# Performance work log

Measured on AMD Instinct MI355X. Metric: run time of the kernel, lower is better.

The kernel has to match this reference:

```python
import jax, jax.numpy as jnp
import numpy as np

TWO_PI = 2.0 * np.pi
EPS = 1e-6


def radians_to_Q(psi, alpha, eta):
    # returns [N,3,3] with columns gamma_1, gamma_2, gamma_3
    ca, sa = jnp.cos(alpha), jnp.sin(alpha)
    ce, se = jnp.cos(eta), jnp.sin(eta)
    cp, sp = jnp.cos(psi), jnp.sin(psi)
    g1 = jnp.stack([ca, sa * ce, sa * se], axis=-1)
    g2 = jnp.stack([-cp * sa, cp * ca * ce - sp * se, cp * ca * se + sp * ce], axis=-1)
    g3 = jnp.stack([sp * sa, -sp * ca * ce - cp * se, -sp * ca * se + cp * ce], axis=-1)
    return jnp.stack([g1, g2, g3], axis=-1)  # [N,3,3], columns are gammas


def log_approximate_c(kappa, beta):
    product = (kappa - 2 * beta) * (kappa + 2 * beta) + EPS
    return jnp.log(TWO_PI) + kappa - 0.5 * jnp.log(product)


def log_del_kappa(kappa, beta):
    num = jnp.log(-TWO_PI * (4 * beta ** 2 + kappa - kappa ** 2)) + kappa
    den = 1.5 * jnp.log(kappa - 2 * beta) + 1.5 * jnp.log(kappa + 2 * beta) + EPS
    return num - den


def log_del_2_kappa(kappa, beta):
    num = jnp.log(TWO_PI * (kappa ** 4 - 2 * kappa ** 3 + (2 - 8 * beta ** 2) * kappa ** 2
                            + 8 * beta ** 2 * kappa + 16 * beta ** 4 + 4 * beta ** 2)) + kappa
    den = 2.5 * jnp.log(kappa - 2 * beta) + 2.5 * jnp.log(kappa + 2 * beta) + EPS
    return num - den


def expected_x(gamma_a1, c, c_k):
    return jnp.exp(c_k - c)[:, None] * gamma_a1  # [N,3]


def expected_xxT(kappa, beta, Q, c, c_k):
    c_kk = log_del_2_kappa(kappa, beta)
    c_beta = log_del_beta(kappa, beta)
    l1 = jnp.exp(c_k - c)
    l2 = 0.5 * (1 - jnp.exp(c_kk - c) + jnp.exp(c_beta - c))
    l3 = 0.5 * (1 - jnp.exp(c_kk - c) - jnp.exp(c_beta - c))
    lam = jnp.stack([l1, l2, l3], axis=-1)  # [N,3]
    # Q diag(lam) Q^T
    return jnp.einsum('nij,nj,nkj->nik', Q, lam, Q)


def log_del_beta(kappa, beta):
    num = jnp.log(8 * np.pi * kappa) + jnp.log(beta)
    den = 1.5 * jnp.log(kappa - 2 * beta) + 1.5 * jnp.log(kappa + 2 * beta) + EPS
    return num - den


def beta_terms(beta_a, gamma_a2, beta_b, gamma_b2, ExxT_a):
    # term_a: beta_a * gamma_a2^T ExxT_a gamma_a2, broadcast over M
    qa = jnp.einsum('ni,nij,nj->n', gamma_a2, ExxT_a, gamma_a2)  # [N]
    term_a = (beta_a * qa)[:, None]  # [N,1] -> broadcast to [N,M]
    # term_b: beta_b * gamma_b2^T ExxT_a gamma_b2 pairwise
    qb = jnp.einsum('mi,nij,mj->nm', gamma_b2, ExxT_a, gamma_b2)  # [N,M]
    term_b = beta_b[None, :] * qb
    M = beta_b.shape[0]
    return jnp.broadcast_to(term_a, (beta_a.shape[0], M)), term_b


def kappa_term(kappa_a, gamma_a1, kappa_b, gamma_b1, Ex_a):
    ka = kappa_a[:, None] * gamma_a1  # [N,3]
    kb = kappa_b[:, None] * gamma_b1  # [M,3]
    # sum over d of (ka[n]-kb[m]) * Ex_a[n]
    return jnp.einsum('nd,nd->n', ka, Ex_a)[:, None] - jnp.einsum('md,nd->nm', kb, Ex_a)


def get_kld(kent_pred, kent_target):
    eta_a, alpha_a, psi_a, kappa_a, beta_a = [kent_pred[:, i] for i in range(5)]
    eta_b, alpha_b, psi_b, kappa_b, beta_b = [kent_target[:, i] for i in range(5)]

    Qa = radians_to_Q(psi_a, alpha_a, eta_a)  # [N,3,3]
    Qb = radians_to_Q(psi_b, alpha_b, eta_b)  # [M,3,3]
    gamma_a1, gamma_a2, gamma_a3 = Qa[:, :, 0], Qa[:, :, 1], Qa[:, :, 2]
    gamma_b1, gamma_b2, gamma_b3 = Qb[:, :, 0], Qb[:, :, 1], Qb[:, :, 2]

    c_a = log_approximate_c(kappa_a, beta_a)
    c_b = log_approximate_c(kappa_b, beta_b)
    c_ka = log_del_kappa(kappa_a, beta_a)

    Ex_a = expected_x(gamma_a1, c_a, c_ka)
    ExxT_a = expected_xxT(kappa_a, beta_a, Qa, c_a, c_ka)

    log_term = c_b[None, :] - c_a[:, None]
    ex_a_term = kappa_term(kappa_a, gamma_a1, kappa_b, gamma_b1, Ex_a)
    ba1, bb1 = beta_terms(beta_a, gamma_a2, beta_b, gamma_b2, ExxT_a)
    ba2, bb2 = beta_terms(beta_a, gamma_a3, beta_b, gamma_b3, ExxT_a)
    return log_term + ex_a_term + ba1 - bb1 - ba2 + bb2


def _make_kent(key, n):
    k1, k2, k3, k4, k5 = jax.random.split(key, 5)
    eta = jax.random.uniform(k1, (n,), minval=-np.pi, maxval=np.pi)
    alpha = jax.random.uniform(k2, (n,), minval=0.0, maxval=np.pi)
    psi = jax.random.uniform(k3, (n,), minval=-np.pi, maxval=np.pi)
    kappa = jax.random.uniform(k4, (n,), minval=10.0, maxval=50.0)
    beta = 0.2 * kappa * jax.random.uniform(k5, (n,), minval=0.5, maxval=1.0)
    return jnp.stack([eta, alpha, psi, kappa, beta], axis=1).astype(jnp.float32)


def setup_inputs() -> dict:
    key = jax.random.key(0)
    kp, kt = jax.random.split(key)
    N = 2048
    M = 2048
    return {"kent_pred": _make_kent(kp, N), "kent_target": _make_kent(kt, M)}


def reference(kent_pred, kent_target):
    return get_kld(kent_pred, kent_target)
```

## Files before the change

kernel.cpp:

```cpp
#include <hip/hip_runtime.h>
#include <math.h>

#define TWO_PI_F 6.2831853071795864769f
#define EPS_F 1e-6f
#define PI_F 3.14159265358979323846f

__device__ __forceinline__ void kent_frame(float eta, float alpha, float psi,
                                           float& g1x, float& g1y, float& g1z,
                                           float& g2x, float& g2y, float& g2z,
                                           float& g3x, float& g3y, float& g3z) {
    float ca = cosf(alpha), sa = sinf(alpha);
    float ce = cosf(eta),   se = sinf(eta);
    float cp = cosf(psi),   sp = sinf(psi);
    g1x = ca;        g1y = sa * ce;                  g1z = sa * se;
    g2x = -cp * sa;  g2y = cp * ca * ce - sp * se;   g2z = cp * ca * se + sp * ce;
    g3x = sp * sa;   g3y = -sp * ca * ce - cp * se;  g3z = -sp * ca * se + cp * ce;
}

__global__ __launch_bounds__(256) void kent_precompute(
    const float* __restrict__ pred, const float* __restrict__ targ,
    float* __restrict__ fw, float* __restrict__ gw, int N, int M)
{
    int i = blockIdx.x * blockDim.x + threadIdx.x;
    if (i < N) {
        const float* r = pred + (size_t)i * 5;
        float eta = r[0], alpha = r[1], psi = r[2], kap = r[3], bet = r[4];
        float g1x,g1y,g1z,g2x,g2y,g2z,g3x,g3y,g3z;
        kent_frame(eta, alpha, psi, g1x,g1y,g1z, g2x,g2y,g2z, g3x,g3y,g3z);

        float km = kap - 2.f*bet, kp = kap + 2.f*bet;
        float lkm = logf(km), lkp = logf(kp);
        float c   = logf(TWO_PI_F) + kap - 0.5f*logf(km*kp + EPS_F);
        float b2 = bet*bet;
        float ck  = logf(TWO_PI_F*(kap*kap - kap - 4.f*b2)) + kap
                  - (1.5f*lkm + 1.5f*lkp + EPS_F);
        float k2 = kap*kap;
        float poly = k2*k2 - 2.f*kap*k2 + (2.f - 8.f*b2)*k2 + 8.f*b2*kap
                   + 16.f*b2*b2 + 4.f*b2;
        float ckk = logf(TWO_PI_F*poly) + kap - (2.5f*lkm + 2.5f*lkp + EPS_F);
        float cbt = logf(8.f*PI_F*kap) + logf(bet) - (1.5f*lkm + 1.5f*lkp + EPS_F);

        float l1  = expf(ck  - c);
        float ekk = expf(ckk - c);
        float eb  = expf(cbt - c);
        float l2 = 0.5f*(1.f - ekk + eb);
        float l3 = 0.5f*(1.f - ekk - eb);

        float Ex = l1*g1x, Ey = l1*g1y, Ez = l1*g1z;
        float S00 = l1*g1x*g1x + l2*g2x*g2x + l3*g3x*g3x;
        float S11 = l1*g1y*g1y + l2*g2y*g2y + l3*g3y*g3y;
        float S22 = l1*g1z*g1z + l2*g2z*g2z + l3*g3z*g3z;
        float S01 = l1*g1x*g1y + l2*g2x*g2y + l3*g3x*g3y;
        float S02 = l1*g1x*g1z + l2*g2x*g2z + l3*g3x*g3z;
        float S12 = l1*g1y*g1z + l2*g2y*g2z + l3*g3y*g3z;

        float qa2 = S00*g2x*g2x + S11*g2y*g2y + S22*g2z*g2z
                  + 2.f*(S01*g2x*g2y + S02*g2x*g2z + S12*g2y*g2z);
        float qa3 = S00*g3x*g3x + S11*g3y*g3y + S22*g3z*g3z
                  + 2.f*(S01*g3x*g3y + S02*g3x*g3z + S12*g3y*g3z);
        float dg1Ex = g1x*Ex + g1y*Ey + g1z*Ez;
        float A = -c + kap*dg1Ex + bet*(qa2 - qa3);

        float* f = fw + (size_t)i * 10;
        f[0]=Ex; f[1]=Ey; f[2]=Ez;
        f[3]=S00; f[4]=S11; f[5]=S22;
        f[6]=2.f*S01; f[7]=2.f*S02; f[8]=2.f*S12;
        f[9]=A;
    } else if (i < N + M) {
        int m = i - N;
        const float* r = targ + (size_t)m * 5;
        float eta = r[0], alpha = r[1], psi = r[2], kap = r[3], bet = r[4];
        float g1x,g1y,g1z,g2x,g2y,g2z,g3x,g3y,g3z;
        kent_frame(eta, alpha, psi, g1x,g1y,g1z, g2x,g2y,g2z, g3x,g3y,g3z);

        float km = kap - 2.f*bet, kp = kap + 2.f*bet;
        float cB = logf(TWO_PI_F) + kap - 0.5f*logf(km*kp + EPS_F);

        float D00 = g2x*g2x - g3x*g3x;
        float D11 = g2y*g2y - g3y*g3y;
        float D22 = g2z*g2z - g3z*g3z;
        float D01 = g2x*g2y - g3x*g3y;
        float D02 = g2x*g2z - g3x*g3z;
        float D12 = g2y*g2z - g3y*g3z;

        gw[0*(size_t)M + m] = kap*g1x;
        gw[1*(size_t)M + m] = kap*g1y;
        gw[2*(size_t)M + m] = kap*g1z;
        gw[3*(size_t)M + m] = bet*D00;
        gw[4*(size_t)M + m] = bet*D11;
        gw[5*(size_t)M + m] = bet*D22;
        gw[6*(size_t)M + m] = bet*D01;
        gw[7*(size_t)M + m] = bet*D02;
        gw[8*(size_t)M + m] = bet*D12;
        gw[9*(size_t)M + m] = cB;
    }
}

__global__ __launch_bounds__(256) void kent_kld_main(
    const float* __restrict__ fw, const float* __restrict__ gw,
    float* __restrict__ out, int N, int M)
{
    int t = threadIdx.x;
    int m0 = blockIdx.x * 1024 + t * 4;
    int n0 = blockIdx.y * 8;
    if (m0 >= M) return;

    if (m0 + 3 < M) {
        float4 G[10];
#pragma unroll
        for (int k = 0; k < 10; ++k)
            G[k] = *(const float4*)(&gw[(size_t)k * M + m0]);
#pragma unroll
        for (int rr = 0; rr < 8; ++rr) {
            int n = n0 + rr;
            if (n >= N) break;
            const float* f = fw + (size_t)n * 10;
            float A = f[9];
            float4 o;
            o.x = A + G[9].x; o.y = A + G[9].y;
            o.z = A + G[9].z; o.w = A + G[9].w;
#pragma unroll
            for (int k = 0; k < 9; ++k) {
                float fk = f[k];
                o.x = fmaf(-fk, G[k].x, o.x);
                o.y = fmaf(-fk, G[k].y, o.y);
                o.z = fmaf(-fk, G[k].z, o.z);
                o.w = fmaf(-fk, G[k].w, o.w);
            }
            *(float4*)(&out[(size_t)n * M + m0]) = o;
        }
    } else {
        for (int mm = m0; mm < M; ++mm) {
            for (int rr = 0; rr < 8; ++rr) {
                int n = n0 + rr;
                if (n >= N) break;
                const float* f = fw + (size_t)n * 10;
                float acc = f[9] + gw[9*(size_t)M + mm];
                for (int k = 0; k < 9; ++k)
                    acc = fmaf(-f[k], gw[(size_t)k * M + mm], acc);
                out[(size_t)n * M + mm] = acc;
            }
        }
    }
}

extern "C" void kernel_launch(void* const* d_in, const int* in_sizes, int n_in,
                              void* d_out, int out_size, void* d_ws, size_t ws_size,
                              hipStream_t stream) {
    const float* pred = (const float*)d_in[0];
    const float* targ = (const float*)d_in[1];
    int N = in_sizes[0] / 5;
    int M = in_sizes[1] / 5;

    float* fw = (float*)d_ws;
    float* gw = fw + (size_t)N * 10;
    float* out = (float*)d_out;

    int total = N + M;
    kent_precompute<<<(total + 255) / 256, 256, 0, stream>>>(pred, targ, fw, gw, N, M);

    dim3 grid((M + 1023) / 1024, (N + 7) / 8);
    kent_kld_main<<<grid, 256, 0, stream>>>(fw, gw, out, N, M);
}
```

Measured before the change: 64.26 us.

## Fuse per-distribution precompute into the pairwise KLD kernel

Merges the separate precompute kernel and the pairwise kernel into one launch. Eight threads per block compute the pred-side coefficients into shared memory. Each thread recomputes the features of its four target distributions in registers instead of reading them from a global workspace. This removes a kernel launch and the workspace write/read round trip, at the cost of recomputing target trig/log features redundantly in every row-block and adding a block-wide barrier.

```diff
diff --git a/kernel.cpp b/kernel.cpp
--- a/kernel.cpp
+++ b/kernel.cpp
@@ -17,13 +17,18 @@
     g3x = sp * sa;   g3y = -sp * ca * ce - cp * se;  g3z = -sp * ca * se + cp * ce;
 }
 
-__global__ __launch_bounds__(256) void kent_precompute(
+__global__ __launch_bounds__(256) void kent_kld_fused(
     const float* __restrict__ pred, const float* __restrict__ targ,
-    float* __restrict__ fw, float* __restrict__ gw, int N, int M)
+    float* __restrict__ out, int N, int M)
 {
-    int i = blockIdx.x * blockDim.x + threadIdx.x;
-    if (i < N) {
-        const float* r = pred + (size_t)i * 5;
+    __shared__ float fsh[8][10];
+
+    int t  = threadIdx.x;
+    int n0 = blockIdx.y * 8;
+    int m0 = blockIdx.x * 1024 + t * 4;
+
+    if (t < 8 && (n0 + t) < N) {
+        const float* r = pred + (size_t)(n0 + t) * 5;
         float eta = r[0], alpha = r[1], psi = r[2], kap = r[3], bet = r[4];
         float g1x,g1y,g1z,g2x,g2y,g2z,g3x,g3y,g3z;
         kent_frame(eta, alpha, psi, g1x,g1y,g1z, g2x,g2y,g2z, g3x,g3y,g3z);
@@ -61,85 +66,67 @@
         float dg1Ex = g1x*Ex + g1y*Ey + g1z*Ez;
         float A = -c + kap*dg1Ex + bet*(qa2 - qa3);
 
-        float* f = fw + (size_t)i * 10;
-        f[0]=Ex; f[1]=Ey; f[2]=Ez;
-        f[3]=S00; f[4]=S11; f[5]=S22;
-        f[6]=2.f*S01; f[7]=2.f*S02; f[8]=2.f*S12;
-        f[9]=A;
-    } else if (i < N + M) {
-        int m = i - N;
-        const float* r = targ + (size_t)m * 5;
-        float eta = r[0], alpha = r[1], psi = r[2], kap = r[3], bet = r[4];
-        float g1x,g1y,g1z,g2x,g2y,g2z,g3x,g3y,g3z;
-        kent_frame(eta, alpha, psi, g1x,g1y,g1z, g2x,g2y,g2z, g3x,g3y,g3z);
+        fsh[t][0]=Ex;      fsh[t][1]=Ey;      fsh[t][2]=Ez;
+        fsh[t][3]=S00;     fsh[t][4]=S11;     fsh[t][5]=S22;
+        fsh[t][6]=2.f*S01; fsh[t][7]=2.f*S02; fsh[t][8]=2.f*S12;
+        fsh[t][9]=A;
+    }
 
-        float km = kap - 2.f*bet, kp = kap + 2.f*bet;
-        float cB = logf(TWO_PI_F) + kap - 0.5f*logf(km*kp + EPS_F);
+    float G[10][4];
+#pragma unroll
+    for (int j = 0; j < 4; ++j) {
+        int m = m0 + j;
+        if (m < M) {
+            const float* r = targ + (size_t)m * 5;
+            float eta = r[0], alpha = r[1], psi = r[2], kap = r[3], bet = r[4];
+            float g1x,g1y,g1z,g2x,g2y,g2z,g3x,g3y,g3z;
+            kent_frame(eta, alpha, psi, g1x,g1y,g1z, g2x,g2y,g2z, g3x,g3y,g3z);
 
-        float D00 = g2x*g2x - g3x*g3x;
-        float D11 = g2y*g2y - g3y*g3y;
-        float D22 = g2z*g2z - g3z*g3z;
-        float D01 = g2x*g2y - g3x*g3y;
-        float D02 = g2x*g2z - g3x*g3z;
-        float D12 = g2y*g2z - g3y*g3z;
+            float km = kap - 2.f*bet, kp = kap + 2.f*bet;
+            float cB = logf(TWO_PI_F) + kap - 0.5f*logf(km*kp + EPS_F);
 
-        gw[0*(size_t)M + m] = kap*g1x;
-        gw[1*(size_t)M + m] = kap*g1y;
-        gw[2*(size_t)M + m] = kap*g1z;
-        gw[3*(size_t)M + m] = bet*D00;
-        gw[4*(size_t)M + m] = bet*D11;
-        gw[5*(size_t)M + m] = bet*D22;
-        gw[6*(size_t)M + m] = bet*D01;
-        gw[7*(size_t)M + m] = bet*D02;
-        gw[8*(size_t)M + m] = bet*D12;
-        gw[9*(size_t)M + m] = cB;
+            G[0][j] = kap*g1x;
+            G[1][j] = kap*g1y;
+            G[2][j] = kap*g1z;
+            G[3][j] = bet*(g2x*g2x - g3x*g3x);
+            G[4][j] = bet*(g2y*g2y - g3y*g3y);
+            G[5][j] = bet*(g2z*g2z - g3z*g3z);
+            G[6][j] = bet*(g2x*g2y - g3x*g3y);
+            G[7][j] = bet*(g2x*g2z - g3x*g3z);
+            G[8][j] = bet*(g2y*g2z - g3y*g3z);
+            G[9][j] = cB;
+        } else {
+#pragma unroll
+            for (int k = 0; k < 10; ++k) G[k][j] = 0.f;
+        }
     }
-}
 
-__global__ __launch_bounds__(256) void kent_kld_main(
-    const float* __restrict__ fw, const float* __restrict__ gw,
-    float* __restrict__ out, int N, int M)
-{
-    int t = threadIdx.x;
-    int m0 = blockIdx.x * 1024 + t * 4;
-    int n0 = blockIdx.y * 8;
+    __syncthreads();
+
     if (m0 >= M) return;
 
-    if (m0 + 3 < M) {
-        float4 G[10];
 #pragma unroll
-        for (int k = 0; k < 10; ++k)
-            G[k] = *(const float4*)(&gw[(size_t)k * M + m0]);
+    for (int rr = 0; rr < 8; ++rr) {
+        int n = n0 + rr;
+        if (n >= N) break;
+        float A = fsh[rr][9];
+        float4 o;
+        o.x = A + G[9][0]; o.y = A + G[9][1];
+        o.z = A + G[9][2]; o.w = A + G[9][3];
 #pragma unroll
-        for (int rr = 0; rr < 8; ++rr) {
-            int n = n0 + rr;
-            if (n >= N) break;
-            const float* f = fw + (size_t)n * 10;
-            float A = f[9];
-            float4 o;
-            o.x = A + G[9].x; o.y = A + G[9].y;
-            o.z = A + G[9].z; o.w = A + G[9].w;
-#pragma unroll
-            for (int k = 0; k < 9; ++k) {
-                float fk = f[k];
-                o.x = fmaf(-fk, G[k].x, o.x);
-                o.y = fmaf(-fk, G[k].y, o.y);
-                o.z = fmaf(-fk, G[k].z, o.z);
-                o.w = fmaf(-fk, G[k].w, o.w);
-            }
+        for (int k = 0; k < 9; ++k) {
+            float fk = fsh[rr][k];
+            o.x = fmaf(-fk, G[k][0], o.x);
+            o.y = fmaf(-fk, G[k][1], o.y);
+            o.z = fmaf(-fk, G[k][2], o.z);
+            o.w = fmaf(-fk, G[k][3], o.w);
+        }
+        if (m0 + 3 < M) {
             *(float4*)(&out[(size_t)n * M + m0]) = o;
-        }
-    } else {
-        for (int mm = m0; mm < M; ++mm) {
-            for (int rr = 0; rr < 8; ++rr) {
-                int n = n0 + rr;
-                if (n >= N) break;
-                const float* f = fw + (size_t)n * 10;
-                float acc = f[9] + gw[9*(size_t)M + mm];
-                for (int k = 0; k < 9; ++k)
-                    acc = fmaf(-f[k], gw[(size_t)k * M + mm], acc);
-                out[(size_t)n * M + mm] = acc;
-            }
+        } else {
+            float ov[4] = {o.x, o.y, o.z, o.w};
+            for (int j = 0; j < 4 && m0 + j < M; ++j)
+                out[(size_t)n * M + m0 + j] = ov[j];
         }
     }
 }
@@ -151,14 +138,8 @@
     const float* targ = (const float*)d_in[1];
     int N = in_sizes[0] / 5;
     int M = in_sizes[1] / 5;
-
-    float* fw = (float*)d_ws;
-    float* gw = fw + (size_t)N * 10;
     float* out = (float*)d_out;
 
-    int total = N + M;
-    kent_precompute<<<(total + 255) / 256, 256, 0, stream>>>(pred, targ, fw, gw, N, M);
-
     dim3 grid((M + 1023) / 1024, (N + 7) / 8);
-    kent_kld_main<<<grid, 256, 0, stream>>>(fw, gw, out, N, M);
+    kent_kld_fused<<<grid, 256, 0, stream>>>(pred, targ, out, N, M);
 }
```

Result: slower. 65.62 us (+2.1%).
